# Kernel tuning notes

Hardware: AMD Instinct MI355X
Metric: run time of the kernel (lower is better)

Reference implementation:

```python
import jax, jax.numpy as jnp
import numpy as np

BLOCKSIZE = 64
# Fixed NF4 codebook (bitsandbytes normal-float 4-bit quantiles)
NF4_CODE = jnp.array([
    -1.0, -0.6961928009986877, -0.5250730514526367, -0.39491748809814453,
    -0.28444138169288635, -0.18477343022823334, -0.09105003625154495, 0.0,
    0.07958029955625534, 0.16093020141124725, 0.24611230194568634,
    0.33791524171829224, 0.44070982933044434, 0.5626170039176941,
    0.7229568362236023, 1.0], dtype=jnp.float32)


def setup_inputs() -> dict:
    key = jax.random.key(0)
    k1, k2, k3, k4 = jax.random.split(key, 4)
    B, IN, OUT = 32, 4096, 14336
    x = jax.random.normal(k1, (B, IN), dtype=jnp.float32)
    codes = jax.random.randint(k2, (OUT, IN), 0, 16, dtype=jnp.int32)
    absmax = jax.random.uniform(k3, (OUT * IN // BLOCKSIZE,), dtype=jnp.float32)
    bias = jax.random.normal(k4, (OUT,), dtype=jnp.float32)
    return {"x": x, "codes": codes, "absmax": absmax, "bias": bias}


def reference(x, codes, absmax, bias):
    out_f, in_f = codes.shape
    # Dequantize: codebook lookup then per-block (64) absmax scaling
    w = NF4_CODE[codes].reshape(-1, BLOCKSIZE) * absmax[:, None]  # [nblocks, 64]
    w = w.reshape(out_f, in_f)
    # y = x @ W^T + bias  (matmul_4bit semantics)
    return jnp.einsum('bi,oi->bo', x, w) + bias
```

## Files before the change

kernel.cpp:

```cpp
#include <hip/hip_runtime.h>
#include <stddef.h>
#include <stdint.h>

#define B_     32
#define IN_    4096
#define OUT_   14336
#define KSPLIT 8
#define KRANGE (IN_ / KSPLIT)
#define NSTEP  (KRANGE / 32)
#define POUT   (B_ * OUT_)

typedef short v8s __attribute__((ext_vector_type(8)));
typedef float v4f __attribute__((ext_vector_type(4)));

__device__ __constant__ float c_nf4[16] = {
    -1.0f, -0.6961928009986877f, -0.5250730514526367f, -0.39491748809814453f,
    -0.28444138169288635f, -0.18477343022823334f, -0.09105003625154495f, 0.0f,
    0.07958029955625534f, 0.16093020141124725f, 0.24611230194568634f,
    0.33791524171829224f, 0.44070982933044434f, 0.5626170039176941f,
    0.7229568362236023f, 1.0f};

__device__ __forceinline__ unsigned f2bf_u(float f) {
    union { float f; unsigned u; } v; v.f = f;
    return (v.u + 0x7FFFu + ((v.u >> 16) & 1u)) >> 16;
}
__device__ __forceinline__ unsigned pack2(float lo, float hi) {
    return f2bf_u(lo) | (f2bf_u(hi) << 16);
}

__global__ __launch_bounds__(256) void prep(const float* __restrict__ x,
                                            unsigned* __restrict__ xB) {
    int t  = blockIdx.x * 256 + threadIdx.x;
    int kt = t >> 7;
    int bt = (t >> 6) & 1;
    int l  = t & 63;
    int b  = bt * 16 + (l & 15);
    int k0 = kt * 32 + (l >> 4) * 8;
    const float* xr = x + (size_t)b * IN_ + k0;
    float4 a = *(const float4*)xr;
    float4 c = *(const float4*)(xr + 4);
    uint4 w;
    w.x = pack2(a.x, a.y);
    w.y = pack2(a.z, a.w);
    w.z = pack2(c.x, c.y);
    w.w = pack2(c.z, c.w);
    *(uint4*)(xB + (size_t)t * 4) = w;
}

__global__ __launch_bounds__(256) void init_out(const float* __restrict__ bias,
                                                float* __restrict__ out) {
    int i4 = (blockIdx.x * 256 + threadIdx.x) * 4;
    int o = i4 % OUT_;
    *(float4*)(out + i4) = *(const float4*)(bias + o);
}

__global__ __launch_bounds__(256) void reduce_out(const float* __restrict__ partial,
                                                  const float* __restrict__ bias,
                                                  float* __restrict__ out) {
    int i4 = (blockIdx.x * 256 + threadIdx.x) * 4;
    int o = i4 % OUT_;
    float4 r = *(const float4*)(bias + o);
#pragma unroll
    for (int s = 0; s < KSPLIT; ++s) {
        float4 p = *(const float4*)(partial + (size_t)s * POUT + i4);
        r.x += p.x; r.y += p.y; r.z += p.z; r.w += p.w;
    }
    *(float4*)(out + i4) = r;
}

template <int ATOMIC>
__global__ __launch_bounds__(256, 4) void nf4_mfma(
    const int* __restrict__ codes, const float* __restrict__ absmax,
    const unsigned* __restrict__ xB, float* __restrict__ dst) {
    __shared__ float lut[16];
    if (threadIdx.x < 16) lut[threadIdx.x] = c_nf4[threadIdx.x];
    __syncthreads();

    const int w  = threadIdx.x >> 6;
    const int l  = threadIdx.x & 63;
    const int ot = blockIdx.x >> 3;
    const int ks = blockIdx.x & 7;
    const int o0 = ot * 64 + w * 16;
    const int m  = l & 15;
    const int q  = l >> 4;

    const int*   crow  = codes + (size_t)(o0 + m) * IN_ + ks * KRANGE + q * 8;
    const float* amrow = absmax + (size_t)(o0 + m) * 64 + ks * (KRANGE / 64);
    const uint4* xbp   = (const uint4*)xB + (size_t)(ks * NSTEP) * 128 + l;

    v4f acc0 = {0.f, 0.f, 0.f, 0.f};
    v4f acc1 = {0.f, 0.f, 0.f, 0.f};

#pragma unroll 4
    for (int kt = 0; kt < NSTEP; ++kt) {
        int4 c0 = *(const int4*)(crow + (size_t)kt * 32);
        int4 c1 = *(const int4*)(crow + (size_t)kt * 32 + 4);
        uint4 b0 = xbp[(size_t)kt * 128];
        uint4 b1 = xbp[(size_t)kt * 128 + 64];
        float am = amrow[kt >> 1];

        union { uint4 u; v8s v; } a, f0, f1;
        a.u.x = pack2(lut[c0.x] * am, lut[c0.y] * am);
        a.u.y = pack2(lut[c0.z] * am, lut[c0.w] * am);
        a.u.z = pack2(lut[c1.x] * am, lut[c1.y] * am);
        a.u.w = pack2(lut[c1.z] * am, lut[c1.w] * am);
        f0.u = b0;
        f1.u = b1;
        acc0 = __builtin_amdgcn_mfma_f32_16x16x32_bf16(a.v, f0.v, acc0, 0, 0, 0);
        acc1 = __builtin_amdgcn_mfma_f32_16x16x32_bf16(a.v, f1.v, acc1, 0, 0, 0);
    }

    const int bc = l & 15;
    const int ob = o0 + q * 4;
#pragma unroll
    for (int r = 0; r < 4; ++r) {
        if (ATOMIC) {
            atomicAdd(dst + (size_t)bc * OUT_ + ob + r, acc0[r]);
            atomicAdd(dst + (size_t)(bc + 16) * OUT_ + ob + r, acc1[r]);
        } else {
            dst[((size_t)ks * B_ + bc) * OUT_ + ob + r]      = acc0[r];
            dst[((size_t)ks * B_ + bc + 16) * OUT_ + ob + r] = acc1[r];
        }
    }
}

extern "C" void kernel_launch(void* const* d_in, const int* in_sizes, int n_in,
                              void* d_out, int out_size, void* d_ws, size_t ws_size,
                              hipStream_t stream) {
    const float* x      = (const float*)d_in[0];
    const int*   codes  = (const int*)d_in[1];
    const float* absmax = (const float*)d_in[2];
    const float* bias   = (const float*)d_in[3];
    float* out = (float*)d_out;
    unsigned* xB = (unsigned*)d_ws;

    prep<<<dim3(64), 256, 0, stream>>>(x, xB);

    const size_t need = 262144 + (size_t)KSPLIT * POUT * 4;
    if (ws_size >= need) {
        float* partial = (float*)((char*)d_ws + 262144);
        nf4_mfma<0><<<dim3(224 * KSPLIT), 256, 0, stream>>>(codes, absmax, xB, partial);
        reduce_out<<<dim3(POUT / 1024), 256, 0, stream>>>(partial, bias, out);
    } else {
        init_out<<<dim3(POUT / 1024), 256, 0, stream>>>(bias, out);
        nf4_mfma<1><<<dim3(224 * KSPLIT), 256, 0, stream>>>(codes, absmax, xB, out);
    }
}
```

Baseline: 334.5 us.

## Stage packed nibble codes in LDS and use fp16 pair-LUT MFMA

Each wave now loads its 16 code rows with coalesced int4 reads, packs them into 4-bit nibbles and stages them in padded shared memory. The inner loop then reads one packed word per lane instead of two strided int4 loads. Dequantization switches from scalar bf16 rounding to a 256-entry fp16 pair lookup table multiplied by a packed fp16 scale, and the matrix multiply uses fp16 MFMA. This removes the per-element bf16 conversion ALU work and the uncoalesced code loads, but gives up the occupancy hint and adds more LDS use. Precision also changes to fp16, so x values beyond the fp16 range could overflow.

```diff
diff --git a/kernel.cpp b/kernel.cpp
--- a/kernel.cpp
+++ b/kernel.cpp
@@ -10,8 +10,9 @@
 #define NSTEP  (KRANGE / 32)
 #define POUT   (B_ * OUT_)
 
-typedef short v8s __attribute__((ext_vector_type(8)));
-typedef float v4f __attribute__((ext_vector_type(4)));
+typedef _Float16 v2h __attribute__((ext_vector_type(2)));
+typedef _Float16 v8h __attribute__((ext_vector_type(8)));
+typedef float    v4f __attribute__((ext_vector_type(4)));
 
 __device__ __constant__ float c_nf4[16] = {
     -1.0f, -0.6961928009986877f, -0.5250730514526367f, -0.39491748809814453f,
@@ -19,14 +20,6 @@
     0.07958029955625534f, 0.16093020141124725f, 0.24611230194568634f,
     0.33791524171829224f, 0.44070982933044434f, 0.5626170039176941f,
     0.7229568362236023f, 1.0f};
-
-__device__ __forceinline__ unsigned f2bf_u(float f) {
-    union { float f; unsigned u; } v; v.f = f;
-    return (v.u + 0x7FFFu + ((v.u >> 16) & 1u)) >> 16;
-}
-__device__ __forceinline__ unsigned pack2(float lo, float hi) {
-    return f2bf_u(lo) | (f2bf_u(hi) << 16);
-}
 
 __global__ __launch_bounds__(256) void prep(const float* __restrict__ x,
                                             unsigned* __restrict__ xB) {
@@ -39,11 +32,12 @@
     const float* xr = x + (size_t)b * IN_ + k0;
     float4 a = *(const float4*)xr;
     float4 c = *(const float4*)(xr + 4);
-    uint4 w;
-    w.x = pack2(a.x, a.y);
-    w.y = pack2(a.z, a.w);
-    w.z = pack2(c.x, c.y);
-    w.w = pack2(c.z, c.w);
+    union { v2h h; unsigned u; } p0, p1, p2, p3;
+    p0.h = (v2h){(_Float16)a.x, (_Float16)a.y};
+    p1.h = (v2h){(_Float16)a.z, (_Float16)a.w};
+    p2.h = (v2h){(_Float16)c.x, (_Float16)c.y};
+    p3.h = (v2h){(_Float16)c.z, (_Float16)c.w};
+    uint4 w = {p0.u, p1.u, p2.u, p3.u};
     *(uint4*)(xB + (size_t)t * 4) = w;
 }
 
@@ -68,23 +62,44 @@
     *(float4*)(out + i4) = r;
 }
 
+#define ROWSTRIDE 67
+
 template <int ATOMIC>
-__global__ __launch_bounds__(256, 4) void nf4_mfma(
+__global__ __launch_bounds__(256) void nf4_mfma(
     const int* __restrict__ codes, const float* __restrict__ absmax,
     const unsigned* __restrict__ xB, float* __restrict__ dst) {
-    __shared__ float lut[16];
-    if (threadIdx.x < 16) lut[threadIdx.x] = c_nf4[threadIdx.x];
+    __shared__ unsigned stage[4 * 16 * ROWSTRIDE];
+    __shared__ v2h lut2[256];
+
+    const int tid = threadIdx.x;
+    {
+        float lo = c_nf4[tid & 15], hi = c_nf4[tid >> 4];
+        lut2[tid] = (v2h){(_Float16)lo, (_Float16)hi};
+    }
     __syncthreads();
 
-    const int w  = threadIdx.x >> 6;
-    const int l  = threadIdx.x & 63;
+    const int w  = tid >> 6;
+    const int l  = tid & 63;
     const int ot = blockIdx.x >> 3;
     const int ks = blockIdx.x & 7;
-    const int o0 = ot * 64 + w * 16;
     const int m  = l & 15;
     const int q  = l >> 4;
+    const int o0 = ot * 64 + w * 16;
 
-    const int*   crow  = codes + (size_t)(o0 + m) * IN_ + ks * KRANGE + q * 8;
+    unsigned* sw = stage + w * 16 * ROWSTRIDE;
+
+#pragma unroll 4
+    for (int i = 0; i < 16; ++i) {
+        const int4* rp = (const int4*)(codes + (size_t)(o0 + i) * IN_ + ks * KRANGE);
+        int4 a0 = rp[2 * l];
+        int4 a1 = rp[2 * l + 1];
+        unsigned pk = (unsigned)(a0.x | (a0.y << 4)) |
+                      ((unsigned)(a0.z | (a0.w << 4)) << 8) |
+                      ((unsigned)(a1.x | (a1.y << 4)) << 16) |
+                      ((unsigned)(a1.z | (a1.w << 4)) << 24);
+        sw[i * ROWSTRIDE + l] = pk;
+    }
+
     const float* amrow = absmax + (size_t)(o0 + m) * 64 + ks * (KRANGE / 64);
     const uint4* xbp   = (const uint4*)xB + (size_t)(ks * NSTEP) * 128 + l;
 
@@ -93,21 +108,24 @@
 
 #pragma unroll 4
     for (int kt = 0; kt < NSTEP; ++kt) {
-        int4 c0 = *(const int4*)(crow + (size_t)kt * 32);
-        int4 c1 = *(const int4*)(crow + (size_t)kt * 32 + 4);
+        unsigned pk = sw[m * ROWSTRIDE + kt * 4 + q];
         uint4 b0 = xbp[(size_t)kt * 128];
         uint4 b1 = xbp[(size_t)kt * 128 + 64];
-        float am = amrow[kt >> 1];
+        float amf = amrow[kt >> 1];
+        _Float16 ah = (_Float16)amf;
+        v2h amh = (v2h){ah, ah};
 
-        union { uint4 u; v8s v; } a, f0, f1;
-        a.u.x = pack2(lut[c0.x] * am, lut[c0.y] * am);
-        a.u.y = pack2(lut[c0.z] * am, lut[c0.w] * am);
-        a.u.z = pack2(lut[c1.x] * am, lut[c1.y] * am);
-        a.u.w = pack2(lut[c1.z] * am, lut[c1.w] * am);
-        f0.u = b0;
-        f1.u = b1;
-        acc0 = __builtin_amdgcn_mfma_f32_16x16x32_bf16(a.v, f0.v, acc0, 0, 0, 0);
-        acc1 = __builtin_amdgcn_mfma_f32_16x16x32_bf16(a.v, f1.v, acc1, 0, 0, 0);
+        union { v2h h[4]; v8h v; } A;
+        A.h[0] = lut2[pk & 255] * amh;
+        A.h[1] = lut2[(pk >> 8) & 255] * amh;
+        A.h[2] = lut2[(pk >> 16) & 255] * amh;
+        A.h[3] = lut2[pk >> 24] * amh;
+
+        union { uint4 u; v8h v; } F0, F1;
+        F0.u = b0;
+        F1.u = b1;
+        acc0 = __builtin_amdgcn_mfma_f32_16x16x32_f16(A.v, F0.v, acc0, 0, 0, 0);
+        acc1 = __builtin_amdgcn_mfma_f32_16x16x32_f16(A.v, F1.v, acc1, 0, 0, 0);
     }
 
     const int bc = l & 15;
```

New measurement: 330.1 us. Within noise of the previous version (-1.3%).
